# Performance work log

Measured on AMD Instinct MI355X. Metric: run time of the kernel, lower is better.

Reference implementation:

```python
import jax, jax.numpy as jnp
import numpy as np

N, E, D = 8192, 4096, 256
EDGE_DENSITY = 0.05  # ~410 nodes per hyperedge; guarantees no empty edge


def _layernorm(x, gamma, beta, eps=1e-5):
    mu = jnp.mean(x, axis=-1, keepdims=True)
    var = jnp.mean((x - mu) ** 2, axis=-1, keepdims=True)
    return (x - mu) * jax.lax.rsqrt(var + eps) * gamma + beta


def setup_inputs() -> dict:
    key = jax.random.key(0)
    k1, k2, k3 = jax.random.split(key, 3)
    node_embeddings = jax.random.normal(k1, (N, D), dtype=jnp.float32)
    # scale 1/sqrt(N) keeps two chained NxN matmuls per layer numerically sane
    target_martrix = jax.random.normal(k2, (N, N), dtype=jnp.float32) / np.float32(np.sqrt(N))
    hypergraph_matrix = (jax.random.uniform(k3, (N, E)) < EDGE_DENSITY).astype(jnp.float32)
    ln_gamma = jnp.ones((D,), jnp.float32)
    ln_beta = jnp.zeros((D,), jnp.float32)
    return {
        "node_embeddings": node_embeddings,
        "target_martrix": target_martrix,
        "hypergraph_matrix": hypergraph_matrix,
        "ln_gamma": ln_gamma,
        "ln_beta": ln_beta,
        "num_layers": 3,
    }


def reference(node_embeddings, target_martrix, hypergraph_matrix, ln_gamma, ln_beta, num_layers):
    # --- propagation: num_layers rounds of A @ x then A.T @ (.), residual + LN ---
    last = node_embeddings
    source = node_embeddings
    for _ in range(num_layers):
        t = target_martrix @ last            # [N, D]
        source = target_martrix.T @ t        # [N, D]  (pre-residual, pre-norm)
        last = _layernorm(source + node_embeddings, ln_gamma, ln_beta)
        # dropout p=0.35 is identity in eval mode
    # --- hyperedge masked-mean + global max (the torch per-edge python loop) ---
    # NOTE: torch loop uses `source_embedding` of the LAST layer (pre-norm).
    Hb = (hypergraph_matrix > 0).astype(source.dtype)   # [N, E]
    sums = Hb.T @ source                                 # [E, D] segment sums
    counts = jnp.sum(Hb, axis=0)[:, None]                # [E, 1] (all > 0 by construction)
    means = sums / counts                                # per-edge masked mean
    return jnp.max(means, axis=0)                        # [D]
```

## Files before the change

kernel.cpp:

```cpp
#include <hip/hip_runtime.h>


typedef __bf16 bf16;
typedef __bf16 bf16x8 __attribute__((ext_vector_type(8)));
typedef float f32x4 __attribute__((ext_vector_type(4)));

__device__ __forceinline__ void gld_lds16(const bf16* g, bf16* l) {
  __builtin_amdgcn_global_load_lds(
      (const __attribute__((address_space(1))) unsigned int*)g,
      (__attribute__((address_space(3))) unsigned int*)l, 16, 0, 0);
}

template <int BN>
__global__ __launch_bounds__(256) void gemm_bt(const bf16* __restrict__ A,
                                               const bf16* __restrict__ B,
                                               float* __restrict__ P,
                                               int N, int K, int Ks) {
  constexpr int BM = 256, BK = 64;
  constexpr int WM = 128, WN = BN / 2;
  constexpr int TM = WM / 16, TN = WN / 16;
  constexpr int QA = BM / 32, QB = BN / 32;

  __shared__ __align__(16) bf16 As[2][BM * BK];
  __shared__ __align__(16) bf16 Bs[2][BN * BK];

  const int t = threadIdx.x, w = t >> 6, l = t & 63;
  const int srow = l >> 3;
  const int schunk = (l & 7) ^ srow;
  const int n0 = blockIdx.x * BN;
  const int kbase = blockIdx.z * Ks;

  const bf16* gA = A + (size_t)(w * 8 + srow) * K + kbase + schunk * 8;
  const bf16* gB = B + (size_t)(n0 + w * 8 + srow) * K + kbase + schunk * 8;

  auto stage = [&](int kk, int buf) {
    const size_t ko = (size_t)kk * BK;
#pragma unroll
    for (int q = 0; q < QA; ++q)
      gld_lds16(gA + (size_t)(q * 32) * K + ko,
                &As[buf][(q * 32 + w * 8) * BK]);
#pragma unroll
    for (int q = 0; q < QB; ++q)
      gld_lds16(gB + (size_t)(q * 32) * K + ko,
                &Bs[buf][(q * 32 + w * 8) * BK]);
  };

  const int lm = l & 15, kq = l >> 4;
  const int wm = (w >> 1) * WM;
  const int wn = (w & 1) * WN;

  f32x4 acc[TM][TN] = {};
  const int nk = Ks / BK;

  stage(0, 0);
  __syncthreads();

  for (int kk = 0; kk < nk; ++kk) {
    const int buf = kk & 1;
    if (kk + 1 < nk) stage(kk + 1, buf ^ 1);
#pragma unroll
    for (int ks = 0; ks < 2; ++ks) {
      const int csw = ((ks * 4 + kq) ^ (lm & 7)) * 8;
      bf16x8 af[TM], bfr[TN];
#pragma unroll
      for (int i = 0; i < TM; ++i)
        af[i] = *(const bf16x8*)(&As[buf][(wm + i * 16 + lm) * BK + csw]);
#pragma unroll
      for (int j = 0; j < TN; ++j)
        bfr[j] = *(const bf16x8*)(&Bs[buf][(wn + j * 16 + lm) * BK + csw]);
#pragma unroll
      for (int i = 0; i < TM; ++i)
#pragma unroll
        for (int j = 0; j < TN; ++j)
          acc[i][j] = __builtin_amdgcn_mfma_f32_16x16x32_bf16(af[i], bfr[j],
                                                              acc[i][j], 0, 0, 0);
    }
    __syncthreads();
  }

  float* Pz = P + (size_t)blockIdx.z * BM * N;
#pragma unroll
  for (int i = 0; i < TM; ++i) {
    const int mrow = wm + i * 16 + kq * 4;
#pragma unroll
    for (int j = 0; j < TN; ++j) {
      const int col = n0 + wn + j * 16 + lm;
#pragma unroll
      for (int r = 0; r < 4; ++r)
        Pz[(size_t)(mrow + r) * N + col] = acc[i][j][r];
    }
  }
}

__global__ __launch_bounds__(256) void reduce4_bf16(const float* __restrict__ P,
                                                    bf16* __restrict__ out,
                                                    size_t MN) {
  const size_t i4 = ((size_t)blockIdx.x * 256 + threadIdx.x) * 4;
  if (i4 >= MN) return;
  f32x4 a = *(const f32x4*)(P + i4);
  f32x4 b = *(const f32x4*)(P + MN + i4);
  f32x4 c = *(const f32x4*)(P + 2 * MN + i4);
  f32x4 d = *(const f32x4*)(P + 3 * MN + i4);
  a = a + b + c + d;
  bf16 o[4] = {(bf16)a[0], (bf16)a[1], (bf16)a[2], (bf16)a[3]};
  *(int2*)(out + i4) = *(const int2*)o;
}

__global__ __launch_bounds__(256) void transpose_conv(
    const float* __restrict__ src, int R, int C, bf16* __restrict__ cpy,
    bf16* __restrict__ trb, float* __restrict__ trf) {
  __shared__ float tile[64][65];
  const int t = threadIdx.x;
  const int col = t & 63, rb4 = t >> 6;
  const int r0 = blockIdx.y * 64, c0 = blockIdx.x * 64;
#pragma unroll
  for (int rr = 0; rr < 64; rr += 4) {
    const int row = rr + rb4;
    const float v = src[(size_t)(r0 + row) * C + c0 + col];
    tile[row][col] = v;
    if (cpy) cpy[(size_t)(r0 + row) * C + c0 + col] = (bf16)v;
  }
  __syncthreads();
#pragma unroll
  for (int rr = 0; rr < 64; rr += 4) {
    const int row = rr + rb4;
    const float v = tile[col][row];
    const size_t di = (size_t)(c0 + row) * R + r0 + col;
    if (trb) trb[di] = (bf16)v;
    if (trf) trf[di] = v;
  }
}

__global__ __launch_bounds__(256) void ln_kernel(const float* __restrict__ P,
                                                 const float* __restrict__ x0t,
                                                 const float* __restrict__ gamma,
                                                 const float* __restrict__ beta,
                                                 bf16* __restrict__ Xt) {
  constexpr size_t MN = (size_t)256 * 8192;
  const int tx = threadIdx.x;
  const int ty = threadIdx.y;
  const int i = blockIdx.x * 32 + tx;
  float vbuf[32];
  float s = 0.f, s2 = 0.f;
#pragma unroll
  for (int dd = 0; dd < 32; ++dd) {
    const int d = ty * 32 + dd;
    const size_t idx = (size_t)d * 8192 + i;
    const float v = P[idx] + P[MN + idx] + P[2 * MN + idx] + P[3 * MN + idx] +
                    x0t[idx];
    vbuf[dd] = v;
    s += v;
    s2 += v * v;
  }
  __shared__ float S[8][32], Q[8][32];
  S[ty][tx] = s;
  Q[ty][tx] = s2;
  __syncthreads();
  __shared__ float MU[32], RS[32];
  if (ty == 0) {
    float a = 0.f, b = 0.f;
#pragma unroll
    for (int r = 0; r < 8; ++r) {
      a += S[r][tx];
      b += Q[r][tx];
    }
    const float mu = a * (1.0f / 256.0f);
    const float var = b * (1.0f / 256.0f) - mu * mu;
    MU[tx] = mu;
    RS[tx] = rsqrtf(var + 1e-5f);
  }
  __syncthreads();
  const float mu = MU[tx], rs = RS[tx];
#pragma unroll
  for (int dd = 0; dd < 32; ++dd) {
    const int d = ty * 32 + dd;
    const float y = (vbuf[dd] - mu) * rs * gamma[d] + beta[d];
    Xt[(size_t)d * 8192 + i] = (bf16)y;
  }
}

__global__ __launch_bounds__(256) void counts_kernel(const bf16* __restrict__ Htb,
                                                     float* __restrict__ invc) {
  const int e = blockIdx.x;
  const bf16* row = Htb + (size_t)e * 8192;
  float s = 0.f;
  for (int i = threadIdx.x; i < 8192; i += 256) s += (float)row[i];
  __shared__ float red[256];
  red[threadIdx.x] = s;
  __syncthreads();
  for (int k = 128; k > 0; k >>= 1) {
    if (threadIdx.x < k) red[threadIdx.x] += red[threadIdx.x + k];
    __syncthreads();
  }
  if (threadIdx.x == 0) invc[e] = 1.0f / red[0];
}

__global__ __launch_bounds__(256) void final_max(const float* __restrict__ P,
                                                 const float* __restrict__ invc,
                                                 float* __restrict__ out,
                                                 int S) {
  constexpr size_t MN = (size_t)256 * 4096;
  const int d = blockIdx.x;
  float m = -3.4e38f;
  for (int e = threadIdx.x; e < 4096; e += 256) {
    const size_t idx = (size_t)d * 4096 + e;
    float s = 0.f;
    for (int z = 0; z < S; ++z) s += P[z * MN + idx];
    m = fmaxf(m, s * invc[e]);
  }
  __shared__ float red[256];
  red[threadIdx.x] = m;
  __syncthreads();
  for (int k = 128; k > 0; k >>= 1) {
    if (threadIdx.x < k)
      red[threadIdx.x] = fmaxf(red[threadIdx.x], red[threadIdx.x + k]);
    __syncthreads();
  }
  if (threadIdx.x == 0) out[d] = red[0];
}

extern "C" void kernel_launch(void* const* d_in, const int* in_sizes, int n_in,
                              void* d_out, int out_size, void* d_ws,
                              size_t ws_size, hipStream_t stream) {
  const float* x0 = (const float*)d_in[0];
  const float* T = (const float*)d_in[1];
  const float* H = (const float*)d_in[2];
  const float* gamma = (const float*)d_in[3];
  const float* beta = (const float*)d_in[4];

  constexpr int Nn = 8192, E = 4096, D = 256, K = 8192;

  char* w = (char*)d_ws;
  size_t off = 0;
  auto carve = [&](size_t bytes) {
    char* p = w + off;
    off += (bytes + 255) & ~(size_t)255;
    return p;
  };
  bf16* Tb = (bf16*)carve((size_t)Nn * Nn * 2);
  bf16* Tt = (bf16*)carve((size_t)Nn * Nn * 2);
  bf16* Htb = (bf16*)carve((size_t)E * Nn * 2);
  float* x0t = (float*)carve((size_t)D * Nn * 4);
  bf16* Xt = (bf16*)carve((size_t)D * Nn * 2);
  bf16* tt = (bf16*)carve((size_t)D * Nn * 2);
  bf16* stb = (bf16*)carve((size_t)D * Nn * 2);
  float* invc = (float*)carve((size_t)E * 4);
  float* P = (float*)carve((size_t)4 * D * Nn * 4);

  if (off > ws_size) {
    hipMemsetAsync(d_out, 0, (size_t)out_size * 4, stream);
    return;
  }

  transpose_conv<<<dim3(128, 128), 256, 0, stream>>>(T, Nn, Nn, Tb, Tt, nullptr);
  transpose_conv<<<dim3(64, 128), 256, 0, stream>>>(H, Nn, E, nullptr, Htb, nullptr);
  transpose_conv<<<dim3(4, 128), 256, 0, stream>>>(x0, Nn, D, nullptr, Xt, x0t);
  counts_kernel<<<E, 256, 0, stream>>>(Htb, invc);

  const size_t MN = (size_t)D * Nn;
  for (int layer = 0; layer < 3; ++layer) {
    gemm_bt<128><<<dim3(64, 1, 4), 256, 0, stream>>>(Xt, Tb, P, Nn, K, K / 4);
    reduce4_bf16<<<(int)(MN / 1024), 256, 0, stream>>>(P, tt, MN);
    gemm_bt<128><<<dim3(64, 1, 4), 256, 0, stream>>>(tt, Tt, P, Nn, K, K / 4);
    if (layer < 2) {
      ln_kernel<<<dim3(256), dim3(32, 8), 0, stream>>>(P, x0t, gamma, beta, Xt);
    } else {
      reduce4_bf16<<<(int)(MN / 1024), 256, 0, stream>>>(P, stb, MN);
    }
  }

  gemm_bt<128><<<dim3(32, 1, 8), 256, 0, stream>>>(stb, Htb, P, E, K, K / 8);
  final_max<<<D, 256, 0, stream>>>(P, invc, (float*)d_out, 8);
}
```

Measured before the change: 1.091 ms.

## Triple-buffer GEMM LDS pipeline and fuse hyperedge counts into transpose

The GEMM moves from double to triple buffering of its LDS tiles. It prefetches two K-tiles ahead and uses a partial vmcnt wait with a single barrier per iteration, replacing two __syncthreads, so global loads overlap more with MFMA work. Separately, the hyperedge counts are now accumulated with atomics inside the H transpose kernel, which removes the separate counts kernel that re-read Htb. The extra LDS buffer (about 144KB total) may limit occupancy, and the vmcnt(12) constant assumes exactly 12 loads per stage.

```diff
diff --git a/kernel.cpp b/kernel.cpp
--- a/kernel.cpp
+++ b/kernel.cpp
@@ -21,8 +21,8 @@
   constexpr int TM = WM / 16, TN = WN / 16;
   constexpr int QA = BM / 32, QB = BN / 32;
 
-  __shared__ __align__(16) bf16 As[2][BM * BK];
-  __shared__ __align__(16) bf16 Bs[2][BN * BK];
+  __shared__ __align__(16) bf16 As[3][BM * BK];
+  __shared__ __align__(16) bf16 Bs[3][BN * BK];
 
   const int t = threadIdx.x, w = t >> 6, l = t & 63;
   const int srow = l >> 3;
@@ -53,11 +53,19 @@
   const int nk = Ks / BK;
 
   stage(0, 0);
-  __syncthreads();
+  if (nk > 1) stage(1, 1);
 
   for (int kk = 0; kk < nk; ++kk) {
-    const int buf = kk & 1;
-    if (kk + 1 < nk) stage(kk + 1, buf ^ 1);
+    if (kk + 1 < nk) {
+      asm volatile("s_waitcnt vmcnt(12)" ::: "memory");
+    } else {
+      asm volatile("s_waitcnt vmcnt(0)" ::: "memory");
+    }
+    __builtin_amdgcn_s_barrier();
+    __builtin_amdgcn_sched_barrier(0);
+    if (kk + 2 < nk) stage(kk + 2, (kk + 2) % 3);
+
+    const int buf = kk % 3;
 #pragma unroll
     for (int ks = 0; ks < 2; ++ks) {
       const int csw = ((ks * 4 + kq) ^ (lm & 7)) * 8;
@@ -75,7 +83,6 @@
           acc[i][j] = __builtin_amdgcn_mfma_f32_16x16x32_bf16(af[i], bfr[j],
                                                               acc[i][j], 0, 0, 0);
     }
-    __syncthreads();
   }
 
   float* Pz = P + (size_t)blockIdx.z * BM * N;
@@ -108,19 +115,28 @@
 
 __global__ __launch_bounds__(256) void transpose_conv(
     const float* __restrict__ src, int R, int C, bf16* __restrict__ cpy,
-    bf16* __restrict__ trb, float* __restrict__ trf) {
+    bf16* __restrict__ trb, float* __restrict__ trf, float* __restrict__ cnt) {
   __shared__ float tile[64][65];
+  __shared__ float cs[4][64];
   const int t = threadIdx.x;
   const int col = t & 63, rb4 = t >> 6;
   const int r0 = blockIdx.y * 64, c0 = blockIdx.x * 64;
+  float csum = 0.f;
 #pragma unroll
   for (int rr = 0; rr < 64; rr += 4) {
     const int row = rr + rb4;
     const float v = src[(size_t)(r0 + row) * C + c0 + col];
     tile[row][col] = v;
+    csum += v;
     if (cpy) cpy[(size_t)(r0 + row) * C + c0 + col] = (bf16)v;
   }
   __syncthreads();
+  if (cnt) {
+    cs[rb4][col] = csum;
+    __syncthreads();
+    if (rb4 == 0)
+      atomicAdd(&cnt[c0 + col], cs[0][col] + cs[1][col] + cs[2][col] + cs[3][col]);
+  }
 #pragma unroll
   for (int rr = 0; rr < 64; rr += 4) {
     const int row = rr + rb4;
@@ -179,24 +195,8 @@
   }
 }
 
-__global__ __launch_bounds__(256) void counts_kernel(const bf16* __restrict__ Htb,
-                                                     float* __restrict__ invc) {
-  const int e = blockIdx.x;
-  const bf16* row = Htb + (size_t)e * 8192;
-  float s = 0.f;
-  for (int i = threadIdx.x; i < 8192; i += 256) s += (float)row[i];
-  __shared__ float red[256];
-  red[threadIdx.x] = s;
-  __syncthreads();
-  for (int k = 128; k > 0; k >>= 1) {
-    if (threadIdx.x < k) red[threadIdx.x] += red[threadIdx.x + k];
-    __syncthreads();
-  }
-  if (threadIdx.x == 0) invc[e] = 1.0f / red[0];
-}
-
 __global__ __launch_bounds__(256) void final_max(const float* __restrict__ P,
-                                                 const float* __restrict__ invc,
+                                                 const float* __restrict__ cnt,
                                                  float* __restrict__ out,
                                                  int S) {
   constexpr size_t MN = (size_t)256 * 4096;
@@ -206,7 +206,7 @@
     const size_t idx = (size_t)d * 4096 + e;
     float s = 0.f;
     for (int z = 0; z < S; ++z) s += P[z * MN + idx];
-    m = fmaxf(m, s * invc[e]);
+    m = fmaxf(m, s / cnt[e]);
   }
   __shared__ float red[256];
   red[threadIdx.x] = m;
@@ -244,7 +244,7 @@
   bf16* Xt = (bf16*)carve((size_t)D * Nn * 2);
   bf16* tt = (bf16*)carve((size_t)D * Nn * 2);
   bf16* stb = (bf16*)carve((size_t)D * Nn * 2);
-  float* invc = (float*)carve((size_t)E * 4);
+  float* cnts = (float*)carve((size_t)E * 4);
   float* P = (float*)carve((size_t)4 * D * Nn * 4);
 
   if (off > ws_size) {
@@ -252,10 +252,13 @@
     return;
   }
 
-  transpose_conv<<<dim3(128, 128), 256, 0, stream>>>(T, Nn, Nn, Tb, Tt, nullptr);
-  transpose_conv<<<dim3(64, 128), 256, 0, stream>>>(H, Nn, E, nullptr, Htb, nullptr);
-  transpose_conv<<<dim3(4, 128), 256, 0, stream>>>(x0, Nn, D, nullptr, Xt, x0t);
-  counts_kernel<<<E, 256, 0, stream>>>(Htb, invc);
+  hipMemsetAsync(cnts, 0, (size_t)E * 4, stream);
+  transpose_conv<<<dim3(128, 128), 256, 0, stream>>>(T, Nn, Nn, Tb, Tt, nullptr,
+                                                     nullptr);
+  transpose_conv<<<dim3(64, 128), 256, 0, stream>>>(H, Nn, E, nullptr, Htb,
+                                                    nullptr, cnts);
+  transpose_conv<<<dim3(4, 128), 256, 0, stream>>>(x0, Nn, D, nullptr, Xt, x0t,
+                                                   nullptr);
 
   const size_t MN = (size_t)D * Nn;
   for (int layer = 0; layer < 3; ++layer) {
@@ -270,5 +273,5 @@
   }
 
   gemm_bt<128><<<dim3(32, 1, 8), 256, 0, stream>>>(stb, Htb, P, E, K, K / 8);
-  final_max<<<D, 256, 0, stream>>>(P, invc, (float*)d_out, 8);
-}
+  final_max<<<D, 256, 0, stream>>>(P, cnts, (float*)d_out, 8);
+}
```

Measured after the change: 1.068 ms. -2.1%, faster.
